# Kernel tuning notes

Hardware: AMD Instinct MI355X
Metric: run time of the kernel (lower is better)

## Reference

```python
import jax, jax.numpy as jnp
import numpy as np

GRID_SIZE = 5
SPLINE_ORDER = 3
NUM_BASIS = GRID_SIZE + SPLINE_ORDER  # 8
BATCH = 4096
POINTS = 512
EMBD = 2048
IN0 = 2 * POINTS - 1  # 1023


def make_grid():
    # torch: arange(-k, G+k+1) * h + grid_range[0], h=(1-(-1))/G=0.4 -> 12 knots
    h = 2.0 / GRID_SIZE
    return jnp.arange(-SPLINE_ORDER, GRID_SIZE + SPLINE_ORDER + 1, dtype=jnp.float32) * h - 1.0


def b_splines(x, grid):
    # x: (N, F) -> bases: (N, F, NUM_BASIS) via Cox-de Boor recursion
    xg = x[..., None]
    bases = ((xg >= grid[:-1]) & (xg < grid[1:])).astype(x.dtype)
    for k in range(1, SPLINE_ORDER + 1):
        left = (xg - grid[:-(k + 1)]) / (grid[k:-1] - grid[:-(k + 1)])
        right = (grid[k + 1:] - xg) / (grid[k + 1:] - grid[1:-k])
        bases = left * bases[..., :-1] + right * bases[..., 1:]
    return bases


def kan_linear(x, base_w, spline_w, scaler, grid):
    # base path: ReLU(x) @ base_w^T  (base_activation=nn.ReLU in KAN)
    base_out = jax.nn.relu(x) @ base_w.T
    # spline path: b_splines(x) blended with scaled spline weights
    bases = b_splines(x, grid)                      # (N, F, K)
    sw = spline_w * scaler[..., None]               # (O, F, K)
    spline_out = jnp.einsum('nfk,ofk->no', bases, sw)
    return base_out + spline_out


def setup_inputs() -> dict:
    key = jax.random.key(0)
    ks = jax.random.split(key, 12)
    dims = [(IN0, EMBD), (EMBD, EMBD), (EMBD, POINTS)]
    inp = {
        'xs': jax.random.uniform(ks[0], (BATCH, POINTS, 1), dtype=jnp.float32),
        'ys': jax.random.uniform(ks[1], (BATCH, POINTS), dtype=jnp.float32),
    }
    i = 2
    for l, (fi, fo) in enumerate(dims):
        s = 1.0 / np.sqrt(fi)
        inp[f'base_w{l}'] = jax.random.normal(ks[i], (fo, fi), dtype=jnp.float32) * s
        inp[f'spline_w{l}'] = jax.random.normal(ks[i + 1], (fo, fi, NUM_BASIS), dtype=jnp.float32) * s
        inp[f'scaler{l}'] = jax.random.normal(ks[i + 2], (fo, fi), dtype=jnp.float32) * s
        i += 3
    return inp


def reference(xs, ys, base_w0, spline_w0, scaler0, base_w1, spline_w1, scaler1,
              base_w2, spline_w2, scaler2):
    grid = make_grid()
    xs2 = xs[:, :, 0]                               # (B, P)
    b = xs2.shape[0]
    # interleave x/y pairs, append final x: (B, 2P-1)
    inter = jnp.stack([xs2[:, :-1], ys[:, :-1]], axis=-1).reshape(b, -1)
    h = jnp.concatenate([inter, xs2[:, -1:]], axis=1)
    h = kan_linear(h, base_w0, spline_w0, scaler0, grid)
    h = kan_linear(h, base_w1, spline_w1, scaler1, grid)
    h = kan_linear(h, base_w2, spline_w2, scaler2, grid)
    return h
```

## Files before the change

### kernel.cpp

```cpp
#include <hip/hip_runtime.h>

#define GLOBAL_AS __attribute__((address_space(1)))
#define LDS_AS    __attribute__((address_space(3)))

typedef __bf16 bf16x8 __attribute__((ext_vector_type(8)));
typedef float  floatx4 __attribute__((ext_vector_type(4)));
typedef unsigned short ushort8 __attribute__((ext_vector_type(8)));

static constexpr int M_BATCH = 4096;
static constexpr int NPTS    = 512;
static constexpr int EMB     = 2048;
static constexpr int F0      = 1023;
static constexpr int F0P     = 1024;
static constexpr int K0      = 9 * F0P;
static constexpr int K12     = 9 * EMB;

__device__ __forceinline__ unsigned short f2bf(float f) {
    unsigned int u = __float_as_uint(f);
    u += 0x7fffu + ((u >> 16) & 1u);
    return (unsigned short)(u >> 16);
}

__device__ __forceinline__ void kan_phi(float x, float* v) {
    float b[11];
    #pragma unroll
    for (int i = 0; i < 11; ++i) {
        const float gl = (float)(i - 3) * 0.4f - 1.0f;
        const float gr = (float)(i - 2) * 0.4f - 1.0f;
        b[i] = (x >= gl && x < gr) ? 1.0f : 0.0f;
    }
    #pragma unroll
    for (int k = 1; k <= 3; ++k) {
        #pragma unroll
        for (int i = 0; i + k < 11; ++i) {
            const float gi   = (float)(i - 3) * 0.4f - 1.0f;
            const float gi1  = (float)(i - 2) * 0.4f - 1.0f;
            const float gik  = (float)(i + k - 3) * 0.4f - 1.0f;
            const float gik1 = (float)(i + k - 2) * 0.4f - 1.0f;
            const float invL = 1.0f / (gik - gi);
            const float invR = 1.0f / (gik1 - gi1);
            b[i] = (x - gi) * invL * b[i] + (gik1 - x) * invR * b[i + 1];
        }
    }
    v[0] = x > 0.0f ? x : 0.0f;
    #pragma unroll
    for (int i = 0; i < 8; ++i) v[1 + i] = b[i];
}

template<int FP, int MODE>
__global__ __launch_bounds__(256)
void aux3_kernel(const float* __restrict__ p0,
                 const float* __restrict__ p1,
                 unsigned short* __restrict__ phi,
                 int F, int NE,
                 const float* __restrict__ bw,
                 const float* __restrict__ sw,
                 const float* __restrict__ sc,
                 unsigned short* __restrict__ wt) {
    __shared__ __align__(16) unsigned short W[9 * FP];
    __shared__ __align__(16) float scL[FP];
    const int tid  = threadIdx.x;
    const int NW8  = (9 * FP) / 8;

    if ((int)blockIdx.x < NE) {
        const int n = blockIdx.x;
        if (MODE == 1) {
            const int half = tid >> 7;
            const int q    = tid & 127;
            const float* src = half ? p1 : p0;
            const float4 v = *reinterpret_cast<const float4*>(
                src + (size_t)n * NPTS + (size_t)q * 4);
            const float xv[4] = {v.x, v.y, v.z, v.w};
            #pragma unroll
            for (int c = 0; c < 4; ++c) {
                const int f = 8 * q + 2 * c + half;
                float ph[9];
                kan_phi(xv[c], ph);
                const bool valid = f < F;
                #pragma unroll
                for (int s = 0; s < 9; ++s)
                    W[f * 9 + s] = valid ? f2bf(ph[s]) : (unsigned short)0;
            }
        } else {
            #pragma unroll
            for (int r = 0; r < 2; ++r) {
                const int q = tid + r * 256;
                const float4 a = *reinterpret_cast<const float4*>(
                    p0 + (size_t)n * F + (size_t)q * 4);
                const float4 c4 = *reinterpret_cast<const float4*>(
                    p1 + (size_t)n * F + (size_t)q * 4);
                const float xv[4] = {a.x + c4.x, a.y + c4.y, a.z + c4.z, a.w + c4.w};
                #pragma unroll
                for (int c = 0; c < 4; ++c) {
                    const int f = q * 4 + c;
                    float ph[9];
                    kan_phi(xv[c], ph);
                    #pragma unroll
                    for (int s = 0; s < 9; ++s)
                        W[f * 9 + s] = f2bf(ph[s]);
                }
            }
        }
        __syncthreads();
        ushort8* dst = reinterpret_cast<ushort8*>(phi + (size_t)n * (size_t)(9 * FP));
        const ushort8* srcW = reinterpret_cast<const ushort8*>(W);
        for (int idx = tid; idx < NW8; idx += 256) dst[idx] = srcW[idx];
    } else {
        const int o = blockIdx.x - NE;
        for (int i = tid; i < FP / 4; i += 256) {
            float4 v;
            if (i * 4 + 4 <= F) {
                v = *reinterpret_cast<const float4*>(sc + (size_t)o * F + (size_t)i * 4);
            } else {
                float tmp[4];
                #pragma unroll
                for (int c = 0; c < 4; ++c)
                    tmp[c] = (i * 4 + c < F) ? sc[(size_t)o * F + i * 4 + c] : 0.0f;
                v = float4{tmp[0], tmp[1], tmp[2], tmp[3]};
            }
            *reinterpret_cast<float4*>(&scL[i * 4]) = v;
        }
        for (int i = tid; i < FP / 4; i += 256) {
            float4 v;
            if (i * 4 + 4 <= F) {
                v = *reinterpret_cast<const float4*>(bw + (size_t)o * F + (size_t)i * 4);
            } else {
                float tmp[4];
                #pragma unroll
                for (int c = 0; c < 4; ++c)
                    tmp[c] = (i * 4 + c < F) ? bw[(size_t)o * F + i * 4 + c] : 0.0f;
                v = float4{tmp[0], tmp[1], tmp[2], tmp[3]};
            }
            const float vv[4] = {v.x, v.y, v.z, v.w};
            #pragma unroll
            for (int c = 0; c < 4; ++c) {
                const int f = i * 4 + c;
                W[f * 9] = (f < F) ? f2bf(vv[c]) : (unsigned short)0;
            }
        }
        __syncthreads();
        for (int i = tid; i < FP * 2; i += 256) {
            const int f = i >> 1;
            const int h = i & 1;
            float4 v = float4{0.f, 0.f, 0.f, 0.f};
            if (i < 2 * F)
                v = *reinterpret_cast<const float4*>(
                    sw + (size_t)o * F * 8 + (size_t)i * 4);
            const float s = scL[f];
            const float vv[4] = {v.x * s, v.y * s, v.z * s, v.w * s};
            #pragma unroll
            for (int c = 0; c < 4; ++c)
                W[f * 9 + 1 + 4 * h + c] = (f < F) ? f2bf(vv[c]) : (unsigned short)0;
        }
        __syncthreads();
        ushort8* dst = reinterpret_cast<ushort8*>(wt + (size_t)o * (size_t)(9 * FP));
        const ushort8* srcW = reinterpret_cast<const ushort8*>(W);
        for (int idx = tid; idx < NW8; idx += 256) dst[idx] = srcW[idx];
    }
}

#define STAGE_H(GB, LB) do { \
    __builtin_amdgcn_global_load_lds((const GLOBAL_AS void*)((GB) + (size_t)r6 * K + scol), \
        (LDS_AS void*)((LB) + wv512), 16, 0, 0); \
    __builtin_amdgcn_global_load_lds((const GLOBAL_AS void*)((GB) + (size_t)(64 + r6) * K + scol), \
        (LDS_AS void*)((LB) + 4096 + wv512), 16, 0, 0); \
} while (0)

__global__ __launch_bounds__(512, 2)
void gemm_bt_256(const unsigned short* __restrict__ A,
                 const unsigned short* __restrict__ B,
                 float* __restrict__ C,
                 int M, int N, int K, int kchunk) {
    __shared__ __align__(16) unsigned short Alds[2 * 16384];
    __shared__ __align__(16) unsigned short Blds[2 * 16384];

    const int tid  = threadIdx.x;
    const int wv   = tid >> 6;
    const int lane = tid & 63;
    const int fr   = lane & 15;
    const int fq   = lane >> 4;
    const int wmi  = wv >> 2;
    const int wni  = wv & 3;

    const int bm = blockIdx.y;
    const int bn = blockIdx.x;
    const int kbase = blockIdx.z * kchunk;
    const int NT = kchunk >> 6;
    float* Cz = C + (size_t)blockIdx.z * (size_t)M * N;

    const int r6    = tid >> 3;
    const int scol  = ((tid & 7) ^ (r6 & 7)) * 8;
    const int wv512 = wv * 512;

    const unsigned short* Ab = A + (size_t)bm * 256 * K;
    const unsigned short* Bb = B + (size_t)bn * 256 * K;

    const int aoff0 = (wmi * 16 + fr) * 64 + ((fq    ) ^ (fr & 7)) * 8;
    const int aoff1 = (wmi * 16 + fr) * 64 + ((4 + fq) ^ (fr & 7)) * 8;
    const int boff0 = (wni * 16 + fr) * 64 + ((fq    ) ^ (fr & 7)) * 8;
    const int boff1 = (wni * 16 + fr) * 64 + ((4 + fq) ^ (fr & 7)) * 8;

    floatx4 zero = {0.f, 0.f, 0.f, 0.f};
    floatx4 acc[8][4];
    #pragma unroll
    for (int i = 0; i < 8; ++i)
        #pragma unroll
        for (int j = 0; j < 4; ++j)
            acc[i][j] = zero;

    {
        const unsigned short* Ag = Ab + kbase;
        const unsigned short* Bg = Bb + kbase;
        STAGE_H(Bg,                   Blds);
        STAGE_H(Ag,                   Alds);
        STAGE_H(Bg + (size_t)128 * K, Blds + 8192);
        STAGE_H(Ag + (size_t)128 * K, Alds + 8192);
        STAGE_H(Bg + 64,                   Blds + 16384);
        STAGE_H(Ag + 64,                   Alds + 16384);
        STAGE_H(Bg + (size_t)128 * K + 64, Blds + 16384 + 8192);
    }
    asm volatile("s_waitcnt vmcnt(6)" ::: "memory");
    __builtin_amdgcn_s_barrier();

    for (int t = 0; t < NT; ++t) {
        unsigned short* Ac = Alds + (t & 1) * 16384;
        unsigned short* Bc = Blds + (t & 1) * 16384;
        const int t1 = (t + 1 < NT) ? t + 1 : NT - 1;
        const int t2 = (t + 2 < NT) ? t + 2 : NT - 1;
        const unsigned short* Ag1 = Ab + kbase + t1 * 64;
        const unsigned short* Ag2 = Ab + kbase + t2 * 64;
        const unsigned short* Bg2 = Bb + kbase + t2 * 64;
        unsigned short* Al1 = Alds + (t1 & 1) * 16384;
        unsigned short* Al2 = Alds + (t2 & 1) * 16384;
        unsigned short* Bl2 = Blds + (t2 & 1) * 16384;

        bf16x8 a_lo[4][2], a_hi[4][2], b_lo[2][2], b_hi[2][2];

        #pragma unroll
        for (int mt = 0; mt < 4; ++mt) {
            a_lo[mt][0] = *reinterpret_cast<const bf16x8*>(Ac + mt * 2048 + aoff0);
            a_lo[mt][1] = *reinterpret_cast<const bf16x8*>(Ac + mt * 2048 + aoff1);
        }
        #pragma unroll
        for (int nt = 0; nt < 2; ++nt) {
            b_lo[nt][0] = *reinterpret_cast<const bf16x8*>(Bc + nt * 4096 + boff0);
            b_lo[nt][1] = *reinterpret_cast<const bf16x8*>(Bc + nt * 4096 + boff1);
        }
        STAGE_H(Ag1 + (size_t)128 * K, Al1 + 8192);
        __builtin_amdgcn_s_setprio(1);
        #pragma unroll
        for (int mt = 0; mt < 4; ++mt)
            #pragma unroll
            for (int nt = 0; nt < 2; ++nt) {
                acc[mt][nt] = __builtin_amdgcn_mfma_f32_16x16x32_bf16(a_lo[mt][0], b_lo[nt][0], acc[mt][nt], 0, 0, 0);
                acc[mt][nt] = __builtin_amdgcn_mfma_f32_16x16x32_bf16(a_lo[mt][1], b_lo[nt][1], acc[mt][nt], 0, 0, 0);
            }
        __builtin_amdgcn_s_setprio(0);
        __builtin_amdgcn_s_barrier();

        #pragma unroll
        for (int nt = 0; nt < 2; ++nt) {
            b_hi[nt][0] = *reinterpret_cast<const bf16x8*>(Bc + (2 + nt) * 4096 + boff0);
            b_hi[nt][1] = *reinterpret_cast<const bf16x8*>(Bc + (2 + nt) * 4096 + boff1);
        }
        STAGE_H(Bg2, Bl2);
        __builtin_amdgcn_s_setprio(1);
        #pragma unroll
        for (int mt = 0; mt < 4; ++mt)
            #pragma unroll
            for (int nt = 0; nt < 2; ++nt) {
                acc[mt][2 + nt] = __builtin_amdgcn_mfma_f32_16x16x32_bf16(a_lo[mt][0], b_hi[nt][0], acc[mt][2 + nt], 0, 0, 0);
                acc[mt][2 + nt] = __builtin_amdgcn_mfma_f32_16x16x32_bf16(a_lo[mt][1], b_hi[nt][1], acc[mt][2 + nt], 0, 0, 0);
            }
        __builtin_amdgcn_s_setprio(0);
        __builtin_amdgcn_s_barrier();

        #pragma unroll
        for (int mt = 0; mt < 4; ++mt) {
            a_hi[mt][0] = *reinterpret_cast<const bf16x8*>(Ac + (4 + mt) * 2048 + aoff0);
            a_hi[mt][1] = *reinterpret_cast<const bf16x8*>(Ac + (4 + mt) * 2048 + aoff1);
        }
        STAGE_H(Ag2, Al2);
        __builtin_amdgcn_s_setprio(1);
        #pragma unroll
        for (int mt = 0; mt < 4; ++mt)
            #pragma unroll
            for (int nt = 0; nt < 2; ++nt) {
                acc[4 + mt][nt] = __builtin_amdgcn_mfma_f32_16x16x32_bf16(a_hi[mt][0], b_lo[nt][0], acc[4 + mt][nt], 0, 0, 0);
                acc[4 + mt][nt] = __builtin_amdgcn_mfma_f32_16x16x32_bf16(a_hi[mt][1], b_lo[nt][1], acc[4 + mt][nt], 0, 0, 0);
            }
        __builtin_amdgcn_s_setprio(0);
        __builtin_amdgcn_s_barrier();

        STAGE_H(Bg2 + (size_t)128 * K, Bl2 + 8192);
        __builtin_amdgcn_s_setprio(1);
        #pragma unroll
        for (int mt = 0; mt < 4; ++mt)
            #pragma unroll
            for (int nt = 0; nt < 2; ++nt) {
                acc[4 + mt][2 + nt] = __builtin_amdgcn_mfma_f32_16x16x32_bf16(a_hi[mt][0], b_hi[nt][0], acc[4 + mt][2 + nt], 0, 0, 0);
                acc[4 + mt][2 + nt] = __builtin_amdgcn_mfma_f32_16x16x32_bf16(a_hi[mt][1], b_hi[nt][1], acc[4 + mt][2 + nt], 0, 0, 0);
            }
        __builtin_amdgcn_s_setprio(0);
        asm volatile("s_waitcnt vmcnt(6)" ::: "memory");
        __builtin_amdgcn_s_barrier();
    }

    #pragma unroll
    for (int mt = 0; mt < 8; ++mt) {
        #pragma unroll
        for (int nt = 0; nt < 4; ++nt) {
            #pragma unroll
            for (int r = 0; r < 4; ++r) {
                int gr = bm * 256 + mt * 32 + wmi * 16 + fq * 4 + r;
                int gc = bn * 256 + nt * 64 + wni * 16 + fr;
                Cz[(size_t)gr * N + gc] = acc[mt][nt][r];
            }
        }
    }
}

__global__ void add8_kernel(const float* __restrict__ p,
                            float* __restrict__ out, int n4, int slice4) {
    int i = blockIdx.x * blockDim.x + threadIdx.x;
    if (i >= n4) return;
    const float4* p4 = reinterpret_cast<const float4*>(p);
    float4 s = p4[i];
    #pragma unroll
    for (int z = 1; z < 8; ++z) {
        float4 v = p4[(size_t)z * slice4 + i];
        s.x += v.x; s.y += v.y; s.z += v.z; s.w += v.w;
    }
    reinterpret_cast<float4*>(out)[i] = s;
}

extern "C" void kernel_launch(void* const* d_in, const int* in_sizes, int n_in,
                              void* d_out, int out_size, void* d_ws, size_t ws_size,
                              hipStream_t stream) {
    const float* xs  = (const float*)d_in[0];
    const float* ys  = (const float*)d_in[1];
    const float* bw0 = (const float*)d_in[2];
    const float* sw0 = (const float*)d_in[3];
    const float* sc0 = (const float*)d_in[4];
    const float* bw1 = (const float*)d_in[5];
    const float* sw1 = (const float*)d_in[6];
    const float* sc1 = (const float*)d_in[7];
    const float* bw2 = (const float*)d_in[8];
    const float* sw2 = (const float*)d_in[9];
    const float* sc2 = (const float*)d_in[10];

    char* ws = (char*)d_ws;
    unsigned short* Phi = (unsigned short*)ws;
    unsigned short* Wt  = (unsigned short*)(ws + 150994944);
    float* Cpart = (float*)(ws + 150994944 + 75497472);
    float* out = (float*)d_out;
    (void)ws_size; (void)in_sizes; (void)n_in; (void)out_size;

    const int T = 256;
    const size_t MN = (size_t)M_BATCH * EMB;

    aux3_kernel<F0P, 1><<<M_BATCH + EMB, T, 0, stream>>>(
        xs, ys, Phi, F0, M_BATCH, bw0, sw0, sc0, Wt);
    gemm_bt_256<<<dim3(8, 16, 2), 512, 0, stream>>>(Phi, Wt, Cpart, M_BATCH, EMB, K0, K0 / 2);

    aux3_kernel<EMB, 0><<<M_BATCH + EMB, T, 0, stream>>>(
        Cpart, Cpart + MN, Phi, EMB, M_BATCH, bw1, sw1, sc1, Wt);
    gemm_bt_256<<<dim3(8, 16, 2), 512, 0, stream>>>(Phi, Wt, Cpart, M_BATCH, EMB, K12, K12 / 2);

    aux3_kernel<EMB, 0><<<M_BATCH + NPTS, T, 0, stream>>>(
        Cpart, Cpart + MN, Phi, EMB, M_BATCH, bw2, sw2, sc2, Wt);
    gemm_bt_256<<<dim3(2, 16, 8), 512, 0, stream>>>(Phi, Wt, Cpart, M_BATCH, NPTS, K12, K12 / 8);
    add8_kernel<<<(M_BATCH * NPTS / 4 + T - 1) / T, T, 0, stream>>>(
        Cpart, out, M_BATCH * NPTS / 4, M_BATCH * NPTS / 4);
}
```

Baseline: 913.0 us.

## Replace Cox-de Boor recursion with closed-form uniform cubic B-spline and split aux kernels

The spline basis is now computed with the closed-form uniform cubic B-spline: the knot interval is found by floor, and only the four nonzero weights are evaluated and written after zero-filling, replacing the full 11-entry Cox-de Boor recursion. The combined activation-expansion/weight-packing kernel is split into two kernels, so each block no longer carries the unused shared buffer and branch of the other role. The goal is less ALU work in the expansion step. The trade is two extra launches per layer and possible floor-boundary rounding differences against the reference near knots.

```diff
diff --git a/kernel.cpp b/kernel.cpp
--- a/kernel.cpp
+++ b/kernel.cpp
@@ -6,6 +6,7 @@
 typedef __bf16 bf16x8 __attribute__((ext_vector_type(8)));
 typedef float  floatx4 __attribute__((ext_vector_type(4)));
 typedef unsigned short ushort8 __attribute__((ext_vector_type(8)));
+typedef unsigned short ushort4v __attribute__((ext_vector_type(4)));
 
 static constexpr int M_BATCH = 4096;
 static constexpr int NPTS    = 512;
@@ -21,142 +22,138 @@
     return (unsigned short)(u >> 16);
 }
 
-__device__ __forceinline__ void kan_phi(float x, float* v) {
-    float b[11];
-    #pragma unroll
-    for (int i = 0; i < 11; ++i) {
-        const float gl = (float)(i - 3) * 0.4f - 1.0f;
-        const float gr = (float)(i - 2) * 0.4f - 1.0f;
-        b[i] = (x >= gl && x < gr) ? 1.0f : 0.0f;
-    }
-    #pragma unroll
-    for (int k = 1; k <= 3; ++k) {
-        #pragma unroll
-        for (int i = 0; i + k < 11; ++i) {
-            const float gi   = (float)(i - 3) * 0.4f - 1.0f;
-            const float gi1  = (float)(i - 2) * 0.4f - 1.0f;
-            const float gik  = (float)(i + k - 3) * 0.4f - 1.0f;
-            const float gik1 = (float)(i + k - 2) * 0.4f - 1.0f;
-            const float invL = 1.0f / (gik - gi);
-            const float invR = 1.0f / (gik1 - gi1);
-            b[i] = (x - gi) * invL * b[i] + (gik1 - x) * invR * b[i + 1];
-        }
-    }
-    v[0] = x > 0.0f ? x : 0.0f;
-    #pragma unroll
-    for (int i = 0; i < 8; ++i) v[1 + i] = b[i];
+__device__ __forceinline__ void emit4(unsigned short* W, int f0,
+                                      const float* xv, int F) {
+    const ushort4v z4 = {0, 0, 0, 0};
+    #pragma unroll
+    for (int j = 0; j < 9; ++j)
+        *reinterpret_cast<ushort4v*>(&W[f0 * 9 + j * 4]) = z4;
+    #pragma unroll
+    for (int c = 0; c < 4; ++c) {
+        const int f = f0 + c;
+        if (f >= F) continue;
+        const float x = xv[c];
+        W[f * 9] = f2bf(x > 0.0f ? x : 0.0f);
+        const int m = (int)floorf((x + 2.2f) * 2.5f);
+        if (m >= 0 && m <= 10) {
+            const float gm = (float)(m - 3) * 0.4f - 1.0f;
+            const float t  = (x - gm) * 2.5f;
+            const float u  = 1.0f - t;
+            const float t2 = t * t, t3 = t2 * t;
+            const float s6 = 1.0f / 6.0f;
+            float Nv[4];
+            Nv[0] = u * u * u * s6;
+            Nv[1] = (3.0f * t3 - 6.0f * t2 + 4.0f) * s6;
+            Nv[2] = (-3.0f * t3 + 3.0f * t2 + 3.0f * t + 1.0f) * s6;
+            Nv[3] = t3 * s6;
+            #pragma unroll
+            for (int r = 0; r < 4; ++r) {
+                const int idx = m - 3 + r;
+                if (idx >= 0 && idx <= 7)
+                    W[f * 9 + 1 + idx] = f2bf(Nv[r]);
+            }
+        }
+    }
 }
 
 template<int FP, int MODE>
 __global__ __launch_bounds__(256)
-void aux3_kernel(const float* __restrict__ p0,
-                 const float* __restrict__ p1,
-                 unsigned short* __restrict__ phi,
-                 int F, int NE,
-                 const float* __restrict__ bw,
-                 const float* __restrict__ sw,
-                 const float* __restrict__ sc,
-                 unsigned short* __restrict__ wt) {
+void expand4_kernel(const float* __restrict__ p0,
+                    const float* __restrict__ p1,
+                    unsigned short* __restrict__ phi, int F) {
+    __shared__ __align__(16) unsigned short W[9 * FP];
+    const int tid = threadIdx.x;
+    const int n   = blockIdx.x;
+    constexpr int NW8 = (9 * FP) / 8;
+
+    if (MODE == 1) {
+        const float2 xsv = *reinterpret_cast<const float2*>(
+            p0 + (size_t)n * NPTS + 2 * tid);
+        const float2 ysv = *reinterpret_cast<const float2*>(
+            p1 + (size_t)n * NPTS + 2 * tid);
+        float xv[4] = {xsv.x, ysv.x, xsv.y, ysv.y};
+        emit4(W, 4 * tid, xv, F);
+    } else {
+        #pragma unroll
+        for (int r = 0; r < FP / 1024; ++r) {
+            const int q = tid + r * 256;
+            const float4 a = *reinterpret_cast<const float4*>(
+                p0 + (size_t)n * F + (size_t)q * 4);
+            const float4 c4 = *reinterpret_cast<const float4*>(
+                p1 + (size_t)n * F + (size_t)q * 4);
+            float xv[4] = {a.x + c4.x, a.y + c4.y, a.z + c4.z, a.w + c4.w};
+            emit4(W, 4 * q, xv, F);
+        }
+    }
+    __syncthreads();
+    ushort8* dst = reinterpret_cast<ushort8*>(phi + (size_t)n * (size_t)(9 * FP));
+    const ushort8* srcW = reinterpret_cast<const ushort8*>(W);
+    #pragma unroll
+    for (int idx = tid; idx < NW8; idx += 256) dst[idx] = srcW[idx];
+}
+
+template<int FP>
+__global__ __launch_bounds__(256)
+void pack4_kernel(const float* __restrict__ bw,
+                  const float* __restrict__ sw,
+                  const float* __restrict__ sc,
+                  unsigned short* __restrict__ wt, int F) {
     __shared__ __align__(16) unsigned short W[9 * FP];
     __shared__ __align__(16) float scL[FP];
-    const int tid  = threadIdx.x;
-    const int NW8  = (9 * FP) / 8;
-
-    if ((int)blockIdx.x < NE) {
-        const int n = blockIdx.x;
-        if (MODE == 1) {
-            const int half = tid >> 7;
-            const int q    = tid & 127;
-            const float* src = half ? p1 : p0;
-            const float4 v = *reinterpret_cast<const float4*>(
-                src + (size_t)n * NPTS + (size_t)q * 4);
-            const float xv[4] = {v.x, v.y, v.z, v.w};
-            #pragma unroll
-            for (int c = 0; c < 4; ++c) {
-                const int f = 8 * q + 2 * c + half;
-                float ph[9];
-                kan_phi(xv[c], ph);
-                const bool valid = f < F;
-                #pragma unroll
-                for (int s = 0; s < 9; ++s)
-                    W[f * 9 + s] = valid ? f2bf(ph[s]) : (unsigned short)0;
-            }
+    const int tid = threadIdx.x;
+    const int o   = blockIdx.x;
+    constexpr int NW8 = (9 * FP) / 8;
+
+    for (int i = tid; i < FP / 4; i += 256) {
+        float4 v;
+        if (i * 4 + 4 <= F) {
+            v = *reinterpret_cast<const float4*>(sc + (size_t)o * F + (size_t)i * 4);
         } else {
-            #pragma unroll
-            for (int r = 0; r < 2; ++r) {
-                const int q = tid + r * 256;
-                const float4 a = *reinterpret_cast<const float4*>(
-                    p0 + (size_t)n * F + (size_t)q * 4);
-                const float4 c4 = *reinterpret_cast<const float4*>(
-                    p1 + (size_t)n * F + (size_t)q * 4);
-                const float xv[4] = {a.x + c4.x, a.y + c4.y, a.z + c4.z, a.w + c4.w};
-                #pragma unroll
-                for (int c = 0; c < 4; ++c) {
-                    const int f = q * 4 + c;
-                    float ph[9];
-                    kan_phi(xv[c], ph);
-                    #pragma unroll
-                    for (int s = 0; s < 9; ++s)
-                        W[f * 9 + s] = f2bf(ph[s]);
-                }
-            }
-        }
-        __syncthreads();
-        ushort8* dst = reinterpret_cast<ushort8*>(phi + (size_t)n * (size_t)(9 * FP));
-        const ushort8* srcW = reinterpret_cast<const ushort8*>(W);
-        for (int idx = tid; idx < NW8; idx += 256) dst[idx] = srcW[idx];
-    } else {
-        const int o = blockIdx.x - NE;
-        for (int i = tid; i < FP / 4; i += 256) {
-            float4 v;
-            if (i * 4 + 4 <= F) {
-                v = *reinterpret_cast<const float4*>(sc + (size_t)o * F + (size_t)i * 4);
-            } else {
-                float tmp[4];
-                #pragma unroll
-                for (int c = 0; c < 4; ++c)
-                    tmp[c] = (i * 4 + c < F) ? sc[(size_t)o * F + i * 4 + c] : 0.0f;
-                v = float4{tmp[0], tmp[1], tmp[2], tmp[3]};
-            }
-            *reinterpret_cast<float4*>(&scL[i * 4]) = v;
-        }
-        for (int i = tid; i < FP / 4; i += 256) {
-            float4 v;
-            if (i * 4 + 4 <= F) {
-                v = *reinterpret_cast<const float4*>(bw + (size_t)o * F + (size_t)i * 4);
-            } else {
-                float tmp[4];
-                #pragma unroll
-                for (int c = 0; c < 4; ++c)
-                    tmp[c] = (i * 4 + c < F) ? bw[(size_t)o * F + i * 4 + c] : 0.0f;
-                v = float4{tmp[0], tmp[1], tmp[2], tmp[3]};
-            }
-            const float vv[4] = {v.x, v.y, v.z, v.w};
-            #pragma unroll
-            for (int c = 0; c < 4; ++c) {
-                const int f = i * 4 + c;
-                W[f * 9] = (f < F) ? f2bf(vv[c]) : (unsigned short)0;
-            }
-        }
-        __syncthreads();
-        for (int i = tid; i < FP * 2; i += 256) {
-            const int f = i >> 1;
-            const int h = i & 1;
-            float4 v = float4{0.f, 0.f, 0.f, 0.f};
-            if (i < 2 * F)
-                v = *reinterpret_cast<const float4*>(
-                    sw + (size_t)o * F * 8 + (size_t)i * 4);
-            const float s = scL[f];
-            const float vv[4] = {v.x * s, v.y * s, v.z * s, v.w * s};
+            float tmp[4];
             #pragma unroll
             for (int c = 0; c < 4; ++c)
-                W[f * 9 + 1 + 4 * h + c] = (f < F) ? f2bf(vv[c]) : (unsigned short)0;
-        }
-        __syncthreads();
-        ushort8* dst = reinterpret_cast<ushort8*>(wt + (size_t)o * (size_t)(9 * FP));
-        const ushort8* srcW = reinterpret_cast<const ushort8*>(W);
-        for (int idx = tid; idx < NW8; idx += 256) dst[idx] = srcW[idx];
-    }
+                tmp[c] = (i * 4 + c < F) ? sc[(size_t)o * F + i * 4 + c] : 0.0f;
+            v = float4{tmp[0], tmp[1], tmp[2], tmp[3]};
+        }
+        *reinterpret_cast<float4*>(&scL[i * 4]) = v;
+    }
+    for (int i = tid; i < FP / 4; i += 256) {
+        float4 v;
+        if (i * 4 + 4 <= F) {
+            v = *reinterpret_cast<const float4*>(bw + (size_t)o * F + (size_t)i * 4);
+        } else {
+            float tmp[4];
+            #pragma unroll
+            for (int c = 0; c < 4; ++c)
+                tmp[c] = (i * 4 + c < F) ? bw[(size_t)o * F + i * 4 + c] : 0.0f;
+            v = float4{tmp[0], tmp[1], tmp[2], tmp[3]};
+        }
+        const float vv[4] = {v.x, v.y, v.z, v.w};
+        #pragma unroll
+        for (int c = 0; c < 4; ++c) {
+            const int f = i * 4 + c;
+            W[f * 9] = (f < F) ? f2bf(vv[c]) : (unsigned short)0;
+        }
+    }
+    __syncthreads();
+    for (int i = tid; i < FP * 2; i += 256) {
+        const int f = i >> 1;
+        const int h = i & 1;
+        float4 v = float4{0.f, 0.f, 0.f, 0.f};
+        if (i < 2 * F)
+            v = *reinterpret_cast<const float4*>(
+                sw + (size_t)o * F * 8 + (size_t)i * 4);
+        const float s = scL[f];
+        const float vv[4] = {v.x * s, v.y * s, v.z * s, v.w * s};
+        #pragma unroll
+        for (int c = 0; c < 4; ++c)
+            W[f * 9 + 1 + 4 * h + c] = (f < F) ? f2bf(vv[c]) : (unsigned short)0;
+    }
+    __syncthreads();
+    ushort8* dst = reinterpret_cast<ushort8*>(wt + (size_t)o * (size_t)(9 * FP));
+    const ushort8* srcW = reinterpret_cast<const ushort8*>(W);
+    #pragma unroll
+    for (int idx = tid; idx < NW8; idx += 256) dst[idx] = srcW[idx];
 }
 
 #define STAGE_H(GB, LB) do { \
@@ -359,16 +356,16 @@
     const int T = 256;
     const size_t MN = (size_t)M_BATCH * EMB;
 
-    aux3_kernel<F0P, 1><<<M_BATCH + EMB, T, 0, stream>>>(
-        xs, ys, Phi, F0, M_BATCH, bw0, sw0, sc0, Wt);
+    expand4_kernel<F0P, 1><<<M_BATCH, T, 0, stream>>>(xs, ys, Phi, F0);
+    pack4_kernel<F0P><<<EMB, T, 0, stream>>>(bw0, sw0, sc0, Wt, F0);
     gemm_bt_256<<<dim3(8, 16, 2), 512, 0, stream>>>(Phi, Wt, Cpart, M_BATCH, EMB, K0, K0 / 2);
 
-    aux3_kernel<EMB, 0><<<M_BATCH + EMB, T, 0, stream>>>(
-        Cpart, Cpart + MN, Phi, EMB, M_BATCH, bw1, sw1, sc1, Wt);
+    expand4_kernel<EMB, 0><<<M_BATCH, T, 0, stream>>>(Cpart, Cpart + MN, Phi, EMB);
+    pack4_kernel<EMB><<<EMB, T, 0, stream>>>(bw1, sw1, sc1, Wt, EMB);
     gemm_bt_256<<<dim3(8, 16, 2), 512, 0, stream>>>(Phi, Wt, Cpart, M_BATCH, EMB, K12, K12 / 2);
 
-    aux3_kernel<EMB, 0><<<M_BATCH + NPTS, T, 0, stream>>>(
-        Cpart, Cpart + MN, Phi, EMB, M_BATCH, bw2, sw2, sc2, Wt);
+    expand4_kernel<EMB, 0><<<M_BATCH, T, 0, stream>>>(Cpart, Cpart + MN, Phi, EMB);
+    pack4_kernel<EMB><<<NPTS, T, 0, stream>>>(bw2, sw2, sc2, Wt, EMB);
     gemm_bt_256<<<dim3(2, 16, 8), 512, 0, stream>>>(Phi, Wt, Cpart, M_BATCH, NPTS, K12, K12 / 8);
     add8_kernel<<<(M_BATCH * NPTS / 4 + T - 1) / T, T, 0, stream>>>(
         Cpart, out, M_BATCH * NPTS / 4, M_BATCH * NPTS / 4);
```

Result: no change. 903.1 us (-1.1%).
